# Kernel tuning notes

Measured on AMD Instinct MI355X. Metric: run time of the kernel, lower is better.

Reference implementation:

```python
import jax, jax.numpy as jnp
import numpy as np

MAT_MODE = ((0, 1), (0, 2), (1, 2))
VEC_MODE = (2, 1, 0)
PE_L = 6


def _sample_plane(plane, gx, gy):
    # plane: [C,H,W]; gx,gy in [-1,1]; bilinear, align_corners=True -> [C,N]
    C, H, W = plane.shape
    ix = (gx + 1.0) * 0.5 * (W - 1)
    iy = (gy + 1.0) * 0.5 * (H - 1)
    ix0 = jnp.clip(jnp.floor(ix).astype(jnp.int32), 0, W - 1)
    iy0 = jnp.clip(jnp.floor(iy).astype(jnp.int32), 0, H - 1)
    ix1 = jnp.minimum(ix0 + 1, W - 1)
    iy1 = jnp.minimum(iy0 + 1, H - 1)
    wx = ix - ix0
    wy = iy - iy0
    v00 = plane[:, iy0, ix0]
    v01 = plane[:, iy0, ix1]
    v10 = plane[:, iy1, ix0]
    v11 = plane[:, iy1, ix1]
    return (v00 * (1 - wx) * (1 - wy) + v01 * wx * (1 - wy)
            + v10 * (1 - wx) * wy + v11 * wx * wy)


def _sample_line(line, g):
    # line: [C,L]; g in [-1,1]; linear interp along L, align_corners=True -> [C,N]
    C, L = line.shape
    iy = (g + 1.0) * 0.5 * (L - 1)
    i0 = jnp.clip(jnp.floor(iy).astype(jnp.int32), 0, L - 1)
    i1 = jnp.minimum(i0 + 1, L - 1)
    w = iy - i0
    return line[:, i0] * (1 - w) + line[:, i1] * w


def _forward(points_3D, ray_unit, density_planes, density_lines,
             color_planes, color_lines, basis_W, W1, b1, W2, b2, W3, b3):
    xyz = jax.lax.stop_gradient(points_3D)  # coords are detached in original
    N = xyz.shape[0]
    # density: sum over 3 axes of (plane_feat * line_feat) summed over comps
    sigma = jnp.zeros((N,), dtype=points_3D.dtype)
    for i in range(3):
        p = _sample_plane(density_planes[i], xyz[:, MAT_MODE[i][0]], xyz[:, MAT_MODE[i][1]])
        l = _sample_line(density_lines[i], xyz[:, VEC_MODE[i]])
        sigma = sigma + jnp.sum(p * l, axis=0)
    # color feature: concat 3x16 comps -> [48,N], multiply, project to 27
    pc = jnp.concatenate([_sample_plane(color_planes[i], xyz[:, MAT_MODE[i][0]], xyz[:, MAT_MODE[i][1]]) for i in range(3)], axis=0)
    lc = jnp.concatenate([_sample_line(color_lines[i], xyz[:, VEC_MODE[i]]) for i in range(3)], axis=0)
    color_feat = (pc * lc).T @ basis_W.T  # [N,27]
    # positional encoding of view dirs, L=6
    freqs = (2.0 ** jnp.arange(PE_L, dtype=points_3D.dtype)) * np.float32(np.pi)
    spec = ray_unit[:, :, None] * freqs  # [N,3,6]
    enc = jnp.stack([jnp.sin(spec), jnp.cos(spec)], axis=-2).reshape(N, -1)  # [N,36]
    feat = jnp.concatenate([color_feat, ray_unit, enc], axis=-1)  # [N,66]
    h = jax.nn.relu(feat @ W1.T + b1)
    h = jax.nn.relu(h @ W2.T + b2)
    rgb = jax.nn.sigmoid(h @ W3.T + b3)
    return rgb, sigma


def setup_inputs():
    key = jax.random.key(0)
    ks = jax.random.split(key, 16)
    N = 1048576
    R = 128   # grid resolution per axis
    C = 16    # components per axis
    CF = 27   # color feature dim
    scale = 0.1
    points_3D = jax.random.uniform(ks[0], (N, 3), dtype=jnp.float32, minval=-1.0, maxval=1.0)
    ray = jax.random.normal(ks[1], (N, 3), dtype=jnp.float32)
    ray_unit = ray / jnp.linalg.norm(ray, axis=-1, keepdims=True)
    density_planes = scale * jax.random.normal(ks[2], (3, C, R, R), dtype=jnp.float32)
    density_lines = scale * jax.random.normal(ks[3], (3, C, R), dtype=jnp.float32)
    color_planes = scale * jax.random.normal(ks[4], (3, C, R, R), dtype=jnp.float32)
    color_lines = scale * jax.random.normal(ks[5], (3, C, R), dtype=jnp.float32)
    basis_W = jax.random.normal(ks[6], (CF, 3 * C), dtype=jnp.float32) * (1.0 / np.sqrt(3 * C))
    in_mlp = 3 + 2 * PE_L * 3 + CF  # 66
    W1 = jax.random.normal(ks[7], (128, in_mlp), dtype=jnp.float32) * (1.0 / np.sqrt(in_mlp))
    b1 = jnp.zeros((128,), dtype=jnp.float32)
    W2 = jax.random.normal(ks[8], (128, 128), dtype=jnp.float32) * (1.0 / np.sqrt(128))
    b2 = jnp.zeros((128,), dtype=jnp.float32)
    W3 = jax.random.normal(ks[9], (3, 128), dtype=jnp.float32) * (1.0 / np.sqrt(128))
    b3 = jnp.zeros((3,), dtype=jnp.float32)
    return {"points_3D": points_3D, "ray_unit": ray_unit,
            "density_planes": density_planes, "density_lines": density_lines,
            "color_planes": color_planes, "color_lines": color_lines,
            "basis_W": basis_W, "W1": W1, "b1": b1, "W2": W2, "b2": b2,
            "W3": W3, "b3": b3}


def reference(points_3D, ray_unit, density_planes, density_lines,
              color_planes, color_lines, basis_W, W1, b1, W2, b2, W3, b3):
    return _forward(points_3D, ray_unit, density_planes, density_lines,
                    color_planes, color_lines, basis_W, W1, b1, W2, b2, W3, b3)
```

## Files before the change

kernel.cpp:

```cpp
#include <hip/hip_runtime.h>

typedef _Float16 f16;
typedef f16 f16x8 __attribute__((ext_vector_type(8)));
typedef f16 f16x2 __attribute__((ext_vector_type(2)));
typedef __fp16 h16x2 __attribute__((ext_vector_type(2)));
typedef float f32x4 __attribute__((ext_vector_type(4)));

#define PI_F 3.14159265358979323846f

constexpr int TP = 128;
constexpr int FSTR = 136;
constexpr int PLANE_ELEMS = 128 * 128 * 16;
constexpr int IPLANE = 128 * 128 * 32;
constexpr int ILINE = 128 * 32;


__global__ void prep_small(const float* __restrict__ W1, const float* __restrict__ basisW,
                           const float* __restrict__ W2, const float* __restrict__ W3,
                           const float* __restrict__ dlines, const float* __restrict__ clines,
                           f16* __restrict__ W1p, f16* __restrict__ W2h, f16* __restrict__ W3p,
                           f16* __restrict__ linesI) {
    int t = blockIdx.x * 256 + threadIdx.x;
    if (t < 128 * 96) {
        int r = t / 96, c = t % 96;
        float v = 0.f;
        if (c < 48) {
            for (int m = 0; m < 27; m++) v += W1[r * 66 + m] * basisW[m * 48 + c];
        } else if (c < 84) {
            v = W1[r * 66 + 30 + (c - 48)];
        } else if (c < 87) {
            v = W1[r * 66 + 27 + (c - 84)];
        }
        W1p[t] = (f16)v;
        return;
    }
    t -= 128 * 96;
    if (t < 128 * 128) {
        int n = t / 128, s = t % 128;
        int k = (s & ~31) + ((s & 31) >> 1) + 16 * (s & 1);
        W2h[t] = (f16)W2[n * 128 + k];
        return;
    }
    t -= 128 * 128;
    if (t < 16 * 128) {
        int r = t / 128, s = t % 128;
        int k = (s & ~31) + ((s & 31) >> 1) + 16 * (s & 1);
        W3p[t] = (f16)(r < 3 ? W3[r * 128 + k] : 0.f);
        return;
    }
    t -= 16 * 128;
    if (t < 3 * ILINE) {
        int axis = t / ILINE;
        int rem = t % ILINE;
        int l = rem / 32, c = rem % 32;
        float v = (c < 16) ? dlines[axis * 2048 + c * 128 + l]
                           : clines[axis * 2048 + (c - 16) * 128 + l];
        linesI[t] = (f16)v;
    }
}

__global__ void interleave_planes(const float* __restrict__ dplanes,
                                  const float* __restrict__ cplanes,
                                  f16* __restrict__ planesI) {
    __shared__ f16 s[128 * 34];
    int b = blockIdx.x;
    int axis = b >> 7;
    int y = b & 127;
    const float* dsrc = dplanes + (size_t)axis * PLANE_ELEMS + y * 128;
    const float* csrc = cplanes + (size_t)axis * PLANE_ELEMS + y * 128;
    int tid = threadIdx.x;
#pragma unroll
    for (int it = 0; it < 8; it++) {
        int c = it * 2 + (tid >> 7);
        int x = tid & 127;
        s[x * 34 + c]      = (f16)dsrc[(size_t)c * 16384 + x];
        s[x * 34 + 16 + c] = (f16)csrc[(size_t)c * 16384 + x];
    }
    __syncthreads();
    f16* dst = planesI + (size_t)(axis * 128 + y) * (128 * 32);
#pragma unroll
    for (int it = 0; it < 8; it++) {
        int d = it * 256 + tid;
        int x = d >> 4, cp = (d & 15) * 2;
        dst[2 * d]     = s[x * 34 + cp];
        dst[2 * d + 1] = s[x * 34 + cp + 1];
    }
}

__global__ __launch_bounds__(256, 4) void nerf_main(
    const float* __restrict__ pts, const float* __restrict__ rayu,
    const f16* __restrict__ planesI, const f16* __restrict__ linesI,
    const f16* __restrict__ W1p, const f16* __restrict__ W2h, const f16* __restrict__ W3p,
    const float* __restrict__ b1, const float* __restrict__ b2, const float* __restrict__ b3,
    float* __restrict__ out, int N) {
    __shared__ __align__(16) f16 tile[TP * FSTR];
    __shared__ __align__(16) float rgbs[TP * 3];
    const int tid = threadIdx.x;
    const int p0 = blockIdx.x * TP;

    const int w = tid >> 6, l = tid & 63, ar = l & 15, kg = l >> 4;
    const int col0 = 32 * w + ar;
    const int col1 = 32 * w + 16 + ar;
    const int wbo = 32 * w + 2 * ar;

    f16x8 w1f0[3], w1f1[3];
#pragma unroll
    for (int k = 0; k < 3; k++) {
        w1f0[k] = *(const f16x8*)(W1p + col0 * 96 + 32 * k + 8 * kg);
        w1f1[k] = *(const f16x8*)(W1p + col1 * 96 + 32 * k + 8 * kg);
    }
    const float bias1_0 = b1[col0], bias1_1 = b1[col1];
    const float bias2_0 = b2[col0], bias2_1 = b2[col1];
    const float bias3v = (ar < 3) ? b3[ar] : 0.f;

    {
        const int grp = tid >> 2;
        const int q = tid & 3;
        const int qc = q - 2;
        const f16* pq = planesI + 8 * q;
        const f16* lq = linesI + 8 * q;
#pragma unroll
        for (int it = 0; it < 2; it++) {
            const int pi = it * 64 + grp;
            const int pp = p0 + pi;
            float g0 = pts[3 * pp + 0], g1 = pts[3 * pp + 1], g2 = pts[3 * pp + 2];
            float g[3] = {g0, g1, g2};
            float sigma = 0.f;
            f16* frow = &tile[pi * FSTR];
#pragma unroll
            for (int i = 0; i < 3; i++) {
                const int m0 = (i == 2) ? 1 : 0;
                const int m1 = (i == 0) ? 1 : 2;
                const int vm = 2 - i;
                float fx = (g[m0] + 1.f) * 63.5f;
                float fy = (g[m1] + 1.f) * 63.5f;
                float fl = (g[vm] + 1.f) * 63.5f;
                int ix0 = min((int)fx, 126);
                int iy0 = min((int)fy, 126);
                int il0 = min((int)fl, 126);
                float wx = fx - (float)ix0, wy = fy - (float)iy0, wl = fl - (float)il0;
                f16 w00 = (f16)((1.f - wx) * (1.f - wy));
                f16 w01 = (f16)(wx * (1.f - wy));
                f16 w10 = (f16)((1.f - wx) * wy);
                f16 w11 = (f16)(wx * wy);
                f16 wl1 = (f16)(1.f - wl), wlh = (f16)wl;
                const f16* c00 = pq + ((i * 128 + iy0) * 128 + ix0) * 32;
                const f16* c10 = c00 + 128 * 32;
                const f16* l0 = lq + (i * 128 + il0) * 32;
                f16x8 v00 = *(const f16x8*)c00;
                f16x8 v01 = *(const f16x8*)(c00 + 32);
                f16x8 v10 = *(const f16x8*)c10;
                f16x8 v11 = *(const f16x8*)(c10 + 32);
                f16x8 pb = v00 * w00 + v01 * w01 + v10 * w10 + v11 * w11;
                f16x8 lv = *(const f16x8*)l0 * wl1 + *(const f16x8*)(l0 + 32) * wlh;
                f16x8 prod = pb * lv;
                if (q < 2) {
                    const f16x2 one2 = {(f16)1.f, (f16)1.f};
#pragma unroll
                    for (int e = 0; e < 4; e++) {
                        f16x2 pr2 = {prod[2 * e], prod[2 * e + 1]};
                        sigma = __builtin_amdgcn_fdot2(pr2, one2, sigma, false);
                    }
                } else {
                    *(f16x8*)(frow + 16 * i + 8 * qc) = prod;
                }
            }
            sigma += __shfl_xor(sigma, 1);
            if (q == 0) out[3 * N + pp] = sigma;
        }
    }

    {
        const int role = tid >> 7;
        const int pi = tid & 127;
        const int pp = p0 + pi;
        f16 tail[24];
        if (role == 0) {
            float r0 = rayu[3 * pp + 0], r1 = rayu[3 * pp + 1];
            float rv[2] = {r0, r1};
#pragma unroll
            for (int d = 0; d < 2; d++) {
                float f = rv[d] * PI_F;
                float s = __sinf(f), c = __cosf(f);
#pragma unroll
                for (int k = 0; k < 6; k++) {
                    tail[12 * d + k] = (f16)s;
                    tail[12 * d + 6 + k] = (f16)c;
                    float ns = 2.f * s * c;
                    float nc = 1.f - 2.f * s * s;
                    s = ns; c = nc;
                }
            }
#pragma unroll
            for (int j = 0; j < 3; j++)
                *(f16x8*)&tile[pi * FSTR + 48 + 8 * j] = *(const f16x8*)&tail[8 * j];
        } else {
            float r0 = rayu[3 * pp + 0], r1 = rayu[3 * pp + 1], r2 = rayu[3 * pp + 2];
            float f = r2 * PI_F;
            float s = __sinf(f), c = __cosf(f);
#pragma unroll
            for (int k = 0; k < 6; k++) {
                tail[k] = (f16)s;
                tail[6 + k] = (f16)c;
                float ns = 2.f * s * c;
                float nc = 1.f - 2.f * s * s;
                s = ns; c = nc;
            }
            tail[12] = (f16)r0; tail[13] = (f16)r1; tail[14] = (f16)r2;
#pragma unroll
            for (int e = 15; e < 24; e++) tail[e] = (f16)0.f;
#pragma unroll
            for (int j = 0; j < 3; j++)
                *(f16x8*)&tile[pi * FSTR + 72 + 8 * j] = *(const f16x8*)&tail[8 * j];
        }
    }
    __syncthreads();

    f32x4 acc[8][2];

#pragma unroll
    for (int m = 0; m < 8; m++) {
        acc[m][0] = (f32x4){bias1_0, bias1_0, bias1_0, bias1_0};
        acc[m][1] = (f32x4){bias1_1, bias1_1, bias1_1, bias1_1};
    }
#pragma unroll
    for (int mb = 0; mb < 2; mb++) {
#pragma unroll
        for (int k = 0; k < 3; k++) {
            f16x8 a[4];
#pragma unroll
            for (int mm = 0; mm < 4; mm++)
                a[mm] = *(const f16x8*)&tile[(16 * (4 * mb + mm) + ar) * FSTR + 32 * k + 8 * kg];
#pragma unroll
            for (int mm = 0; mm < 4; mm++) {
                int m = 4 * mb + mm;
                acc[m][0] = __builtin_amdgcn_mfma_f32_16x16x32_f16(a[mm], w1f0[k], acc[m][0], 0, 0, 0);
                acc[m][1] = __builtin_amdgcn_mfma_f32_16x16x32_f16(a[mm], w1f1[k], acc[m][1], 0, 0, 0);
            }
        }
    }

    f16x8 w2f0[4], w2f1[4];
#pragma unroll
    for (int k = 0; k < 4; k++) {
        w2f0[k] = *(const f16x8*)(W2h + col0 * 128 + 32 * k + 8 * kg);
        w2f1[k] = *(const f16x8*)(W2h + col1 * 128 + 32 * k + 8 * kg);
    }

    __syncthreads();
#pragma unroll
    for (int m = 0; m < 8; m++)
#pragma unroll
        for (int j = 0; j < 4; j++) {
            int row = 16 * m + 4 * kg + j;
            h16x2 pr = __builtin_amdgcn_cvt_pkrtz(fmaxf(acc[m][0][j], 0.f),
                                                  fmaxf(acc[m][1][j], 0.f));
            *(h16x2*)&tile[row * FSTR + wbo] = pr;
        }
    __syncthreads();

#pragma unroll
    for (int m = 0; m < 8; m++) {
        acc[m][0] = (f32x4){bias2_0, bias2_0, bias2_0, bias2_0};
        acc[m][1] = (f32x4){bias2_1, bias2_1, bias2_1, bias2_1};
    }
#pragma unroll
    for (int mb = 0; mb < 2; mb++) {
#pragma unroll
        for (int k = 0; k < 4; k++) {
            f16x8 a[4];
#pragma unroll
            for (int mm = 0; mm < 4; mm++)
                a[mm] = *(const f16x8*)&tile[(16 * (4 * mb + mm) + ar) * FSTR + 32 * k + 8 * kg];
#pragma unroll
            for (int mm = 0; mm < 4; mm++) {
                int m = 4 * mb + mm;
                acc[m][0] = __builtin_amdgcn_mfma_f32_16x16x32_f16(a[mm], w2f0[k], acc[m][0], 0, 0, 0);
                acc[m][1] = __builtin_amdgcn_mfma_f32_16x16x32_f16(a[mm], w2f1[k], acc[m][1], 0, 0, 0);
            }
        }
    }

    f16x8 w3f[4];
#pragma unroll
    for (int k = 0; k < 4; k++)
        w3f[k] = *(const f16x8*)(W3p + ar * 128 + 32 * k + 8 * kg);

    __syncthreads();
#pragma unroll
    for (int m = 0; m < 8; m++)
#pragma unroll
        for (int j = 0; j < 4; j++) {
            int row = 16 * m + 4 * kg + j;
            h16x2 pr = __builtin_amdgcn_cvt_pkrtz(fmaxf(acc[m][0][j], 0.f),
                                                  fmaxf(acc[m][1][j], 0.f));
            *(h16x2*)&tile[row * FSTR + wbo] = pr;
        }
    __syncthreads();

    {
        f32x4 a3[2];
#pragma unroll
        for (int mm = 0; mm < 2; mm++) a3[mm] = (f32x4){bias3v, bias3v, bias3v, bias3v};
#pragma unroll
        for (int k = 0; k < 4; k++) {
#pragma unroll
            for (int mm = 0; mm < 2; mm++) {
                int m = 2 * w + mm;
                f16x8 a = *(const f16x8*)&tile[(16 * m + ar) * FSTR + 32 * k + 8 * kg];
                a3[mm] = __builtin_amdgcn_mfma_f32_16x16x32_f16(a, w3f[k], a3[mm], 0, 0, 0);
            }
        }
        if (ar < 3) {
#pragma unroll
            for (int mm = 0; mm < 2; mm++) {
                int m = 2 * w + mm;
#pragma unroll
                for (int j = 0; j < 4; j++) {
                    int row = 16 * m + 4 * kg + j;
                    rgbs[3 * row + ar] = 1.f / (1.f + __expf(-a3[mm][j]));
                }
            }
        }
    }
    __syncthreads();

    if (tid < 96) {
        float4 v = *(const float4*)&rgbs[4 * tid];
        *(float4*)&out[3 * p0 + 4 * tid] = v;
    }
}

extern "C" void kernel_launch(void* const* d_in, const int* in_sizes, int n_in,
                              void* d_out, int out_size, void* d_ws, size_t ws_size,
                              hipStream_t stream) {
    const float* pts    = (const float*)d_in[0];
    const float* rayu   = (const float*)d_in[1];
    const float* dplanes = (const float*)d_in[2];
    const float* dlines  = (const float*)d_in[3];
    const float* cplanes = (const float*)d_in[4];
    const float* clines  = (const float*)d_in[5];
    const float* basisW  = (const float*)d_in[6];
    const float* W1 = (const float*)d_in[7];
    const float* b1 = (const float*)d_in[8];
    const float* W2 = (const float*)d_in[9];
    const float* b2 = (const float*)d_in[10];
    const float* W3 = (const float*)d_in[11];
    const float* b3 = (const float*)d_in[12];
    float* out = (float*)d_out;
    const int N = in_sizes[0] / 3;

    f16* planesI = (f16*)d_ws;
    f16* linesI = planesI + 3 * IPLANE;
    f16* W1p = linesI + 3 * ILINE;
    f16* W2h = W1p + 128 * 96;
    f16* W3p = W2h + 128 * 128;

    prep_small<<<168, 256, 0, stream>>>(W1, basisW, W2, W3, dlines, clines,
                                        W1p, W2h, W3p, linesI);
    interleave_planes<<<384, 256, 0, stream>>>(dplanes, cplanes, planesI);
    nerf_main<<<N / TP, 256, 0, stream>>>(pts, rayu, planesI, linesI,
                                          W1p, W2h, W3p, b1, b2, b3, out, N);
}
```

Baseline: 134.1 us.

## Make each wave own 32 points end-to-end and drop block barriers

Each wave now handles its own 32 rows through sampling, encoding and all three MLP layers. Because no wave reads another wave's rows, every __syncthreads is removed. The weights are no longer held in registers for the whole block; each wave streams W1/W2 fragments per output block from global/L2. MFMA sections run under raised s_setprio, and the final rgb is written straight to global instead of being staged through shared memory. The trade-off is extra weight-load traffic per wave and less coalesced output stores, in exchange for no block-wide synchronisation and better overlap between waves.

```diff
diff --git a/kernel.cpp b/kernel.cpp
--- a/kernel.cpp
+++ b/kernel.cpp
@@ -94,34 +94,20 @@
     const float* __restrict__ b1, const float* __restrict__ b2, const float* __restrict__ b3,
     float* __restrict__ out, int N) {
     __shared__ __align__(16) f16 tile[TP * FSTR];
-    __shared__ __align__(16) float rgbs[TP * 3];
     const int tid = threadIdx.x;
     const int p0 = blockIdx.x * TP;
-
-    const int w = tid >> 6, l = tid & 63, ar = l & 15, kg = l >> 4;
-    const int col0 = 32 * w + ar;
-    const int col1 = 32 * w + 16 + ar;
-    const int wbo = 32 * w + 2 * ar;
-
-    f16x8 w1f0[3], w1f1[3];
-#pragma unroll
-    for (int k = 0; k < 3; k++) {
-        w1f0[k] = *(const f16x8*)(W1p + col0 * 96 + 32 * k + 8 * kg);
-        w1f1[k] = *(const f16x8*)(W1p + col1 * 96 + 32 * k + 8 * kg);
-    }
-    const float bias1_0 = b1[col0], bias1_1 = b1[col1];
-    const float bias2_0 = b2[col0], bias2_1 = b2[col1];
-    const float bias3v = (ar < 3) ? b3[ar] : 0.f;
-
-    {
-        const int grp = tid >> 2;
-        const int q = tid & 3;
+    const int w = tid >> 6, lane = tid & 63, ar = lane & 15, kg = lane >> 4;
+    const int rowb = 32 * w;
+
+    {
+        const int grp = lane >> 2;
+        const int q = lane & 3;
         const int qc = q - 2;
         const f16* pq = planesI + 8 * q;
         const f16* lq = linesI + 8 * q;
 #pragma unroll
         for (int it = 0; it < 2; it++) {
-            const int pi = it * 64 + grp;
+            const int pi = rowb + 16 * it + grp;
             const int pp = p0 + pi;
             float g0 = pts[3 * pp + 0], g1 = pts[3 * pp + 1], g2 = pts[3 * pp + 2];
             float g[3] = {g0, g1, g2};
@@ -171,8 +157,8 @@
     }
 
     {
-        const int role = tid >> 7;
-        const int pi = tid & 127;
+        const int role = lane >> 5;
+        const int pi = rowb + (lane & 31);
         const int pp = p0 + pi;
         f16 tail[24];
         if (role == 0) {
@@ -191,9 +177,6 @@
                     s = ns; c = nc;
                 }
             }
-#pragma unroll
-            for (int j = 0; j < 3; j++)
-                *(f16x8*)&tile[pi * FSTR + 48 + 8 * j] = *(const f16x8*)&tail[8 * j];
         } else {
             float r0 = rayu[3 * pp + 0], r1 = rayu[3 * pp + 1], r2 = rayu[3 * pp + 2];
             float f = r2 * PI_F;
@@ -209,125 +192,133 @@
             tail[12] = (f16)r0; tail[13] = (f16)r1; tail[14] = (f16)r2;
 #pragma unroll
             for (int e = 15; e < 24; e++) tail[e] = (f16)0.f;
-#pragma unroll
-            for (int j = 0; j < 3; j++)
-                *(f16x8*)&tile[pi * FSTR + 72 + 8 * j] = *(const f16x8*)&tail[8 * j];
-        }
-    }
-    __syncthreads();
-
-    f32x4 acc[8][2];
-
-#pragma unroll
-    for (int m = 0; m < 8; m++) {
-        acc[m][0] = (f32x4){bias1_0, bias1_0, bias1_0, bias1_0};
-        acc[m][1] = (f32x4){bias1_1, bias1_1, bias1_1, bias1_1};
-    }
-#pragma unroll
-    for (int mb = 0; mb < 2; mb++) {
-#pragma unroll
-        for (int k = 0; k < 3; k++) {
-            f16x8 a[4];
-#pragma unroll
-            for (int mm = 0; mm < 4; mm++)
-                a[mm] = *(const f16x8*)&tile[(16 * (4 * mb + mm) + ar) * FSTR + 32 * k + 8 * kg];
-#pragma unroll
-            for (int mm = 0; mm < 4; mm++) {
-                int m = 4 * mb + mm;
-                acc[m][0] = __builtin_amdgcn_mfma_f32_16x16x32_f16(a[mm], w1f0[k], acc[m][0], 0, 0, 0);
-                acc[m][1] = __builtin_amdgcn_mfma_f32_16x16x32_f16(a[mm], w1f1[k], acc[m][1], 0, 0, 0);
-            }
-        }
-    }
-
-    f16x8 w2f0[4], w2f1[4];
-#pragma unroll
-    for (int k = 0; k < 4; k++) {
-        w2f0[k] = *(const f16x8*)(W2h + col0 * 128 + 32 * k + 8 * kg);
-        w2f1[k] = *(const f16x8*)(W2h + col1 * 128 + 32 * k + 8 * kg);
-    }
-
-    __syncthreads();
-#pragma unroll
-    for (int m = 0; m < 8; m++)
-#pragma unroll
-        for (int j = 0; j < 4; j++) {
-            int row = 16 * m + 4 * kg + j;
-            h16x2 pr = __builtin_amdgcn_cvt_pkrtz(fmaxf(acc[m][0][j], 0.f),
-                                                  fmaxf(acc[m][1][j], 0.f));
-            *(h16x2*)&tile[row * FSTR + wbo] = pr;
-        }
-    __syncthreads();
-
-#pragma unroll
-    for (int m = 0; m < 8; m++) {
-        acc[m][0] = (f32x4){bias2_0, bias2_0, bias2_0, bias2_0};
-        acc[m][1] = (f32x4){bias2_1, bias2_1, bias2_1, bias2_1};
-    }
-#pragma unroll
-    for (int mb = 0; mb < 2; mb++) {
-#pragma unroll
-        for (int k = 0; k < 4; k++) {
-            f16x8 a[4];
-#pragma unroll
-            for (int mm = 0; mm < 4; mm++)
-                a[mm] = *(const f16x8*)&tile[(16 * (4 * mb + mm) + ar) * FSTR + 32 * k + 8 * kg];
-#pragma unroll
-            for (int mm = 0; mm < 4; mm++) {
-                int m = 4 * mb + mm;
-                acc[m][0] = __builtin_amdgcn_mfma_f32_16x16x32_f16(a[mm], w2f0[k], acc[m][0], 0, 0, 0);
-                acc[m][1] = __builtin_amdgcn_mfma_f32_16x16x32_f16(a[mm], w2f1[k], acc[m][1], 0, 0, 0);
-            }
-        }
-    }
-
-    f16x8 w3f[4];
-#pragma unroll
-    for (int k = 0; k < 4; k++)
-        w3f[k] = *(const f16x8*)(W3p + ar * 128 + 32 * k + 8 * kg);
-
-    __syncthreads();
-#pragma unroll
-    for (int m = 0; m < 8; m++)
-#pragma unroll
-        for (int j = 0; j < 4; j++) {
-            int row = 16 * m + 4 * kg + j;
-            h16x2 pr = __builtin_amdgcn_cvt_pkrtz(fmaxf(acc[m][0][j], 0.f),
-                                                  fmaxf(acc[m][1][j], 0.f));
-            *(h16x2*)&tile[row * FSTR + wbo] = pr;
-        }
-    __syncthreads();
-
-    {
-        f32x4 a3[2];
-#pragma unroll
-        for (int mm = 0; mm < 2; mm++) a3[mm] = (f32x4){bias3v, bias3v, bias3v, bias3v};
-#pragma unroll
-        for (int k = 0; k < 4; k++) {
-#pragma unroll
-            for (int mm = 0; mm < 2; mm++) {
-                int m = 2 * w + mm;
-                f16x8 a = *(const f16x8*)&tile[(16 * m + ar) * FSTR + 32 * k + 8 * kg];
-                a3[mm] = __builtin_amdgcn_mfma_f32_16x16x32_f16(a, w3f[k], a3[mm], 0, 0, 0);
-            }
-        }
+        }
+#pragma unroll
+        for (int j = 0; j < 3; j++)
+            *(f16x8*)&tile[pi * FSTR + 48 + 24 * role + 8 * j] = *(const f16x8*)&tail[8 * j];
+    }
+
+    {
+        f16x8 a1[2][3];
+#pragma unroll
+        for (int mt = 0; mt < 2; mt++)
+#pragma unroll
+            for (int k = 0; k < 3; k++)
+                a1[mt][k] = *(const f16x8*)&tile[(rowb + 16 * mt + ar) * FSTR + 32 * k + 8 * kg];
+#pragma unroll
+        for (int nb = 0; nb < 4; nb++) {
+            f16x8 bf[2][3];
+            float bias[2];
+#pragma unroll
+            for (int h = 0; h < 2; h++) {
+                int n = 2 * nb + h;
+#pragma unroll
+                for (int k = 0; k < 3; k++)
+                    bf[h][k] = *(const f16x8*)(W1p + (16 * n + ar) * 96 + 32 * k + 8 * kg);
+                bias[h] = b1[16 * n + ar];
+            }
+            f32x4 acc[2][2];
+#pragma unroll
+            for (int mt = 0; mt < 2; mt++)
+#pragma unroll
+                for (int h = 0; h < 2; h++)
+                    acc[mt][h] = (f32x4){bias[h], bias[h], bias[h], bias[h]};
+            __builtin_amdgcn_s_setprio(1);
+#pragma unroll
+            for (int k = 0; k < 3; k++)
+#pragma unroll
+                for (int h = 0; h < 2; h++)
+#pragma unroll
+                    for (int mt = 0; mt < 2; mt++)
+                        acc[mt][h] = __builtin_amdgcn_mfma_f32_16x16x32_f16(a1[mt][k], bf[h][k], acc[mt][h], 0, 0, 0);
+            __builtin_amdgcn_s_setprio(0);
+#pragma unroll
+            for (int mt = 0; mt < 2; mt++)
+#pragma unroll
+                for (int j = 0; j < 4; j++) {
+                    h16x2 pr = __builtin_amdgcn_cvt_pkrtz(fmaxf(acc[mt][0][j], 0.f),
+                                                          fmaxf(acc[mt][1][j], 0.f));
+                    *(h16x2*)&tile[(rowb + 16 * mt + 4 * kg + j) * FSTR + 32 * nb + 2 * ar] = pr;
+                }
+        }
+    }
+
+    {
+        f16x8 a2[2][4];
+#pragma unroll
+        for (int mt = 0; mt < 2; mt++)
+#pragma unroll
+            for (int k = 0; k < 4; k++)
+                a2[mt][k] = *(const f16x8*)&tile[(rowb + 16 * mt + ar) * FSTR + 32 * k + 8 * kg];
+#pragma unroll
+        for (int nb = 0; nb < 4; nb++) {
+            f16x8 bf[2][4];
+            float bias[2];
+#pragma unroll
+            for (int h = 0; h < 2; h++) {
+                int n = 2 * nb + h;
+#pragma unroll
+                for (int k = 0; k < 4; k++)
+                    bf[h][k] = *(const f16x8*)(W2h + (16 * n + ar) * 128 + 32 * k + 8 * kg);
+                bias[h] = b2[16 * n + ar];
+            }
+            f32x4 acc[2][2];
+#pragma unroll
+            for (int mt = 0; mt < 2; mt++)
+#pragma unroll
+                for (int h = 0; h < 2; h++)
+                    acc[mt][h] = (f32x4){bias[h], bias[h], bias[h], bias[h]};
+            __builtin_amdgcn_s_setprio(1);
+#pragma unroll
+            for (int k = 0; k < 4; k++)
+#pragma unroll
+                for (int h = 0; h < 2; h++)
+#pragma unroll
+                    for (int mt = 0; mt < 2; mt++)
+                        acc[mt][h] = __builtin_amdgcn_mfma_f32_16x16x32_f16(a2[mt][k], bf[h][k], acc[mt][h], 0, 0, 0);
+            __builtin_amdgcn_s_setprio(0);
+#pragma unroll
+            for (int mt = 0; mt < 2; mt++)
+#pragma unroll
+                for (int j = 0; j < 4; j++) {
+                    h16x2 pr = __builtin_amdgcn_cvt_pkrtz(fmaxf(acc[mt][0][j], 0.f),
+                                                          fmaxf(acc[mt][1][j], 0.f));
+                    *(h16x2*)&tile[(rowb + 16 * mt + 4 * kg + j) * FSTR + 32 * nb + 2 * ar] = pr;
+                }
+        }
+    }
+
+    {
+        f16x8 a3[2][4];
+#pragma unroll
+        for (int mt = 0; mt < 2; mt++)
+#pragma unroll
+            for (int k = 0; k < 4; k++)
+                a3[mt][k] = *(const f16x8*)&tile[(rowb + 16 * mt + ar) * FSTR + 32 * k + 8 * kg];
+        f16x8 w3f[4];
+#pragma unroll
+        for (int k = 0; k < 4; k++)
+            w3f[k] = *(const f16x8*)(W3p + ar * 128 + 32 * k + 8 * kg);
+        const float bias3v = (ar < 3) ? b3[ar] : 0.f;
+        f32x4 a3acc[2];
+#pragma unroll
+        for (int mt = 0; mt < 2; mt++) a3acc[mt] = (f32x4){bias3v, bias3v, bias3v, bias3v};
+        __builtin_amdgcn_s_setprio(1);
+#pragma unroll
+        for (int k = 0; k < 4; k++)
+#pragma unroll
+            for (int mt = 0; mt < 2; mt++)
+                a3acc[mt] = __builtin_amdgcn_mfma_f32_16x16x32_f16(a3[mt][k], w3f[k], a3acc[mt], 0, 0, 0);
+        __builtin_amdgcn_s_setprio(0);
         if (ar < 3) {
 #pragma unroll
-            for (int mm = 0; mm < 2; mm++) {
-                int m = 2 * w + mm;
+            for (int mt = 0; mt < 2; mt++)
 #pragma unroll
                 for (int j = 0; j < 4; j++) {
-                    int row = 16 * m + 4 * kg + j;
-                    rgbs[3 * row + ar] = 1.f / (1.f + __expf(-a3[mm][j]));
-                }
-            }
-        }
-    }
-    __syncthreads();
-
-    if (tid < 96) {
-        float4 v = *(const float4*)&rgbs[4 * tid];
-        *(float4*)&out[3 * p0 + 4 * tid] = v;
+                    int row = p0 + rowb + 16 * mt + 4 * kg + j;
+                    out[3 * row + ar] = 1.f / (1.f + __expf(-a3acc[mt][j]));
+                }
+        }
     }
 }
 
```

New measurement: 230.7 us. +72.0%, slower.
